# Performance work log

Hardware: AMD Instinct MI355X
Metric: run time of the kernel (lower is better)

The kernel has to match this reference:

```python
import jax, jax.numpy as jnp
import numpy as np

B, DIM_IN, DIM_OUT = 2048, 4096, 4096


def setup_inputs() -> dict:
    key = jax.random.key(0)
    k1, k2, k3 = jax.random.split(key, 3)
    # binary input activations (0/1), stored as int32
    x = jax.random.randint(k1, (B, DIM_IN), 0, 2, dtype=jnp.int32)
    masks = jax.random.uniform(k2, (DIM_IN, DIM_OUT)) < 0.5
    # integer thresholds in [0, dim_in)
    thresholds = jax.random.randint(k3, (DIM_OUT,), 0, DIM_IN, dtype=jnp.int32)
    return {"x": x, "masks": masks, "thresholds": thresholds}


def reference(x, masks, thresholds):
    # Original: expand x to (B, dim_in, dim_out), XNOR with masks, sum over dim_in,
    # compare vs thresholds. XNOR(a,b) = a*b + (1-a)*(1-b), so the sum over dim_in
    # is two GEMMs -- never materialize the (B, dim_in, dim_out) tensor.
    xf = x.astype(jnp.float32)              # (B, dim_in), values in {0,1}
    mf = masks.astype(jnp.float32)          # (dim_in, dim_out)
    sums = xf @ mf + (1.0 - xf) @ (1.0 - mf)  # (B, dim_out), popcount of agreements
    return sums > thresholds.astype(jnp.float32)[None, :]  # (B, dim_out) bool
```

## Files before the change

### kernel.cpp

```cpp
#include <hip/hip_runtime.h>
#include <stdint.h>

#define BB    2048
#define DIN   4096
#define DOUT  4096


using v4i  = __attribute__((ext_vector_type(4)))  int;
using v16i = __attribute__((ext_vector_type(16))) int;

__device__ __forceinline__ void async_load16(const void* g, void* l) {
    __builtin_amdgcn_global_load_lds(
        (const __attribute__((address_space(1))) unsigned int*)g,
        (__attribute__((address_space(3))) unsigned int*)l,
        16, 0, 0);
}

__device__ __forceinline__ unsigned int to_pm1(unsigned int c) {
    return c + ((c ^ 0x01010101u) * 255u);
}

__global__ void pack_all(const int* __restrict__ x,
                         const void* __restrict__ mraw,
                         char* __restrict__ x8p,
                         char* __restrict__ b8p) {
    const int tid = threadIdx.x;
    if (blockIdx.x < 256) {
        const int br  = blockIdx.x & 31;
        const int bp  = blockIdx.x >> 5;
        const int row = br * 64 + (tid & 63);
        const int w   = tid >> 6;
        #pragma unroll
        for (int j = 0; j < 8; ++j) {
            const int p = bp * 32 + w * 8 + j;
            const int4* src = (const int4*)(x + (size_t)row * DIN + p * 16);
            int4 a0 = src[0], a1 = src[1], a2 = src[2], a3 = src[3];
            uint4 v;
            v.x = to_pm1((unsigned)(a0.x & 1) | ((unsigned)(a0.y & 1) << 8) |
                         ((unsigned)(a0.z & 1) << 16) | ((unsigned)(a0.w & 1) << 24));
            v.y = to_pm1((unsigned)(a1.x & 1) | ((unsigned)(a1.y & 1) << 8) |
                         ((unsigned)(a1.z & 1) << 16) | ((unsigned)(a1.w & 1) << 24));
            v.z = to_pm1((unsigned)(a2.x & 1) | ((unsigned)(a2.y & 1) << 8) |
                         ((unsigned)(a2.z & 1) << 16) | ((unsigned)(a2.w & 1) << 24));
            v.w = to_pm1((unsigned)(a3.x & 1) | ((unsigned)(a3.y & 1) << 8) |
                         ((unsigned)(a3.z & 1) << 16) | ((unsigned)(a3.w & 1) << 24));
            *(uint4*)(x8p + ((size_t)p * 2048 + row) * 16) = v;
        }
    } else {
        const int bw = blockIdx.x - 256;
        const int k0 = (bw & 63) * 64;
        const int n0 = (bw >> 6) * 64;

        const unsigned char* mb = (const unsigned char*)mraw;
        int myv = (mb[tid] != 0) + (mb[tid + 256] != 0) +
                  (mb[tid + 512] != 0) + (mb[tid + 768] != 0);
        #pragma unroll
        for (int d = 32; d; d >>= 1) myv += __shfl_xor(myv, d);
        const bool isU8 = (myv > 64);

        const int n4 = (tid & 15) * 4;
        const int k4 = (tid >> 4) * 4;
        unsigned int a[4];
        if (isU8) {
            #pragma unroll
            for (int r = 0; r < 4; ++r)
                a[r] = *(const unsigned int*)(mb + (size_t)(k0 + k4 + r) * DOUT + n0 + n4);
        } else {
            const int4* m32 = (const int4*)mraw;
            #pragma unroll
            for (int r = 0; r < 4; ++r) {
                int4 v = m32[((size_t)(k0 + k4 + r) * DOUT + n0 + n4) >> 2];
                a[r] = (unsigned int)(v.x & 1) |
                       ((unsigned int)(v.y & 1) << 8) |
                       ((unsigned int)(v.z & 1) << 16) |
                       ((unsigned int)(v.w & 1) << 24);
            }
        }
        unsigned int x0 = __builtin_amdgcn_perm(a[1], a[0], 0x05010400u);
        unsigned int x1 = __builtin_amdgcn_perm(a[3], a[2], 0x05010400u);
        unsigned int x2 = __builtin_amdgcn_perm(a[1], a[0], 0x07030602u);
        unsigned int x3 = __builtin_amdgcn_perm(a[3], a[2], 0x07030602u);
        unsigned int c0 = __builtin_amdgcn_perm(x1, x0, 0x05040100u);
        unsigned int c1 = __builtin_amdgcn_perm(x1, x0, 0x07060302u);
        unsigned int c2 = __builtin_amdgcn_perm(x3, x2, 0x05040100u);
        unsigned int c3 = __builtin_amdgcn_perm(x3, x2, 0x07060302u);
        const int p   = (k0 + k4) >> 4;
        const int off = k4 & 15;
        *(unsigned int*)(b8p + ((size_t)p * 4096 + n0 + n4 + 0) * 16 + off) = to_pm1(c0);
        *(unsigned int*)(b8p + ((size_t)p * 4096 + n0 + n4 + 1) * 16 + off) = to_pm1(c1);
        *(unsigned int*)(b8p + ((size_t)p * 4096 + n0 + n4 + 2) * 16 + off) = to_pm1(c2);
        *(unsigned int*)(b8p + ((size_t)p * 4096 + n0 + n4 + 3) * 16 + off) = to_pm1(c3);
    }
}

__global__ __launch_bounds__(256)
void bgemm(const char* __restrict__ x8p,
           const char* __restrict__ b8p,
           const int* __restrict__ thr,
           int* __restrict__ out) {
    const int flat = blockIdx.y * 32 + blockIdx.x;
    const int xcd  = flat & 7;
    const int idx  = flat >> 3;
    const int bm   = (xcd & 1) * 8 + (idx & 7);
    const int bn   = (xcd >> 1) * 8 + (idx >> 3);
    const int m0   = bm * 128;
    const int o0   = bn * 128;

    const int tid  = threadIdx.x;
    const int lane = tid & 63;
    const int wv   = tid >> 6;
    const int wm   = (wv & 1) * 64;
    const int wn   = (wv >> 1) * 64;
    const int l31  = lane & 31;
    const int lh   = lane >> 5;

    __shared__ __align__(16) char lA[2][8 * 128 * 16];
    __shared__ __align__(16) char lB[2][8 * 128 * 16];

    auto stage = [&](int c, int buf) {
        #pragma unroll
        for (int pp = 0; pp < 2; ++pp) {
            const int pl = 2 * wv + pp;
            const int pg = 8 * c + pl;
            #pragma unroll
            for (int h = 0; h < 2; ++h) {
                const int r = h * 64 + lane;
                async_load16(x8p + ((size_t)pg * 2048 + m0 + r) * 16,
                             &lA[buf][(pl * 128 + r) * 16]);
                async_load16(b8p + ((size_t)pg * 4096 + o0 + r) * 16,
                             &lB[buf][(pl * 128 + r) * 16]);
            }
        }
    };

    v16i acc[2][2];
    #pragma unroll
    for (int t = 0; t < 2; ++t)
        #pragma unroll
        for (int u = 0; u < 2; ++u)
            acc[t][u] = (v16i)(0);

    stage(0, 0);
    __syncthreads();

    for (int c = 0; c < 32; ++c) {
        const int buf = c & 1;
        if (c < 31) stage(c + 1, buf ^ 1);

        #pragma unroll
        for (int ks = 0; ks < 4; ++ks) {
            const int poff = (2 * ks + lh) * 2048;
            v4i aF[2], bF[2];
            #pragma unroll
            for (int t = 0; t < 2; ++t) {
                aF[t] = *(const v4i*)&lA[buf][poff + (wm + t * 32 + l31) * 16];
                bF[t] = *(const v4i*)&lB[buf][poff + (wn + t * 32 + l31) * 16];
            }
            acc[0][0] = __builtin_amdgcn_mfma_i32_32x32x32_i8(aF[0], bF[0], acc[0][0], 0, 0, 0);
            acc[0][1] = __builtin_amdgcn_mfma_i32_32x32x32_i8(aF[0], bF[1], acc[0][1], 0, 0, 0);
            acc[1][0] = __builtin_amdgcn_mfma_i32_32x32x32_i8(aF[1], bF[0], acc[1][0], 0, 0, 0);
            acc[1][1] = __builtin_amdgcn_mfma_i32_32x32x32_i8(aF[1], bF[1], acc[1][1], 0, 0, 0);
        }
        __syncthreads();
    }

    #pragma unroll
    for (int u = 0; u < 2; ++u) {
        const int o   = o0 + wn + u * 32 + l31;
        const int lim = 2 * thr[o] - DIN;
        #pragma unroll
        for (int t = 0; t < 2; ++t) {
            #pragma unroll
            for (int r = 0; r < 16; ++r) {
                const int rowl = (r & 3) + 8 * (r >> 2) + 4 * lh;
                const int b    = m0 + wm + t * 32 + rowl;
                out[(size_t)b * DOUT + o] = (acc[t][u][r] > lim) ? 1 : 0;
            }
        }
    }
}

extern "C" void kernel_launch(void* const* d_in, const int* in_sizes, int n_in,
                              void* d_out, int out_size, void* d_ws, size_t ws_size,
                              hipStream_t stream) {
    const int* x          = (const int*)d_in[0];
    const void* masks     = d_in[1];
    const int* thresholds = (const int*)d_in[2];
    int* out              = (int*)d_out;

    char* x8p = (char*)d_ws;
    char* b8p = (char*)d_ws + ((size_t)8 << 20);

    pack_all<<<256 + 4096, 256, 0, stream>>>(x, masks, x8p, b8p);
    bgemm<<<dim3(32, 16), 256, 0, stream>>>(x8p, b8p, thresholds, out);
}
```

Measured before the change: 177.9 us.

## Load MFMA fragments directly from global memory with register prefetch, drop LDS staging

Removes the LDS double-buffered staging in the binary GEMM. Each wave now loads its MFMA operand fragments straight from global memory into registers through a 4-deep software prefetch ring, and there are no block barriers. Launch bounds now request 2 blocks per CU. This removes LDS traffic and __syncthreads stalls, but the waves of a block no longer share loads, so global/L2 traffic is duplicated and more vector registers are live.

```diff
diff --git a/kernel.cpp b/kernel.cpp
--- a/kernel.cpp
+++ b/kernel.cpp
@@ -8,13 +8,6 @@
 
 using v4i  = __attribute__((ext_vector_type(4)))  int;
 using v16i = __attribute__((ext_vector_type(16))) int;
-
-__device__ __forceinline__ void async_load16(const void* g, void* l) {
-    __builtin_amdgcn_global_load_lds(
-        (const __attribute__((address_space(1))) unsigned int*)g,
-        (__attribute__((address_space(3))) unsigned int*)l,
-        16, 0, 0);
-}
 
 __device__ __forceinline__ unsigned int to_pm1(unsigned int c) {
     return c + ((c ^ 0x01010101u) * 255u);
@@ -93,7 +86,7 @@
     }
 }
 
-__global__ __launch_bounds__(256)
+__global__ __launch_bounds__(256, 2)
 void bgemm(const char* __restrict__ x8p,
            const char* __restrict__ b8p,
            const int* __restrict__ thr,
@@ -114,24 +107,14 @@
     const int l31  = lane & 31;
     const int lh   = lane >> 5;
 
-    __shared__ __align__(16) char lA[2][8 * 128 * 16];
-    __shared__ __align__(16) char lB[2][8 * 128 * 16];
-
-    auto stage = [&](int c, int buf) {
-        #pragma unroll
-        for (int pp = 0; pp < 2; ++pp) {
-            const int pl = 2 * wv + pp;
-            const int pg = 8 * c + pl;
-            #pragma unroll
-            for (int h = 0; h < 2; ++h) {
-                const int r = h * 64 + lane;
-                async_load16(x8p + ((size_t)pg * 2048 + m0 + r) * 16,
-                             &lA[buf][(pl * 128 + r) * 16]);
-                async_load16(b8p + ((size_t)pg * 4096 + o0 + r) * 16,
-                             &lB[buf][(pl * 128 + r) * 16]);
-            }
-        }
-    };
+    const char* pA[2];
+    const char* pB[2];
+    #pragma unroll
+    for (int t = 0; t < 2; ++t)
+        pA[t] = x8p + ((size_t)lh * 2048 + m0 + wm + t * 32 + l31) * 16;
+    #pragma unroll
+    for (int u = 0; u < 2; ++u)
+        pB[u] = b8p + ((size_t)lh * 4096 + o0 + wn + u * 32 + l31) * 16;
 
     v16i acc[2][2];
     #pragma unroll
@@ -140,29 +123,32 @@
         for (int u = 0; u < 2; ++u)
             acc[t][u] = (v16i)(0);
 
-    stage(0, 0);
-    __syncthreads();
+    v4i aF[4][2], bF[4][2];
+    auto loadf = [&](int ks, int buf) {
+        #pragma unroll
+        for (int t = 0; t < 2; ++t)
+            aF[buf][t] = *(const v4i*)(pA[t] + (size_t)ks * 65536);
+        #pragma unroll
+        for (int u = 0; u < 2; ++u)
+            bF[buf][u] = *(const v4i*)(pB[u] + (size_t)ks * 131072);
+    };
+    auto mfmas = [&](int buf) {
+        acc[0][0] = __builtin_amdgcn_mfma_i32_32x32x32_i8(aF[buf][0], bF[buf][0], acc[0][0], 0, 0, 0);
+        acc[0][1] = __builtin_amdgcn_mfma_i32_32x32x32_i8(aF[buf][0], bF[buf][1], acc[0][1], 0, 0, 0);
+        acc[1][0] = __builtin_amdgcn_mfma_i32_32x32x32_i8(aF[buf][1], bF[buf][0], acc[1][0], 0, 0, 0);
+        acc[1][1] = __builtin_amdgcn_mfma_i32_32x32x32_i8(aF[buf][1], bF[buf][1], acc[1][1], 0, 0, 0);
+    };
 
-    for (int c = 0; c < 32; ++c) {
-        const int buf = c & 1;
-        if (c < 31) stage(c + 1, buf ^ 1);
-
-        #pragma unroll
-        for (int ks = 0; ks < 4; ++ks) {
-            const int poff = (2 * ks + lh) * 2048;
-            v4i aF[2], bF[2];
-            #pragma unroll
-            for (int t = 0; t < 2; ++t) {
-                aF[t] = *(const v4i*)&lA[buf][poff + (wm + t * 32 + l31) * 16];
-                bF[t] = *(const v4i*)&lB[buf][poff + (wn + t * 32 + l31) * 16];
-            }
-            acc[0][0] = __builtin_amdgcn_mfma_i32_32x32x32_i8(aF[0], bF[0], acc[0][0], 0, 0, 0);
-            acc[0][1] = __builtin_amdgcn_mfma_i32_32x32x32_i8(aF[0], bF[1], acc[0][1], 0, 0, 0);
-            acc[1][0] = __builtin_amdgcn_mfma_i32_32x32x32_i8(aF[1], bF[0], acc[1][0], 0, 0, 0);
-            acc[1][1] = __builtin_amdgcn_mfma_i32_32x32x32_i8(aF[1], bF[1], acc[1][1], 0, 0, 0);
-        }
-        __syncthreads();
+    #pragma unroll
+    for (int ks = 0; ks < 4; ++ks) loadf(ks, ks);
+    #pragma unroll 4
+    for (int ks = 0; ks < 124; ++ks) {
+        const int buf = ks & 3;
+        mfmas(buf);
+        loadf(ks + 4, buf);
     }
+    #pragma unroll
+    for (int ks = 124; ks < 128; ++ks) mfmas(ks & 3);
 
     #pragma unroll
     for (int u = 0; u < 2; ++u) {
```

New measurement: 177.8 us. No clear change (-0.0%).
